# Kernel tuning notes

Hardware: AMD Instinct MI355X
Metric: run time of the kernel (lower is better)

The kernel has to match this reference:

```python
import jax, jax.numpy as jnp
import numpy as np

B, P = 16, 1024
D_TIME, NUM_MODS = 8, 22
DIM_S = NUM_MODS + D_TIME + 1  # 31
PHI_W, N_HEADS, DP = 32, 4, 32
PSI_W, PSI_L, RHO_W = 64, 64, 64
SQRT_DP = float(np.sqrt(DP))


def setup_inputs() -> dict:
    key = jax.random.key(0)
    ks = jax.random.split(key, 16)
    rn = lambda k, shape: jax.random.normal(k, shape, jnp.float32) * 0.05
    return dict(
        times=jax.random.uniform(ks[0], (B, P), jnp.float32) * 48.0,
        values=jax.random.normal(ks[1], (B, P), jnp.float32),
        measurements=jax.random.randint(ks[2], (B, P), 0, NUM_MODS + 1),
        non_pad_mask=jnp.ones((B, P, 1), jnp.float32),
        W_psi1=rn(ks[3], (DIM_S, PSI_W)), b_psi1=jnp.zeros((PSI_W,), jnp.float32),
        W_psi2=rn(ks[4], (PSI_W, PSI_L)), b_psi2=jnp.zeros((PSI_L,), jnp.float32),
        W_key=rn(ks[5], (DIM_S + PSI_L, N_HEADS * DP)), b_key=jnp.zeros((N_HEADS * DP,), jnp.float32),
        query=rn(ks[6], (N_HEADS, DP)),
        W_phi1=rn(ks[7], (DIM_S, PHI_W)), b_phi1=jnp.zeros((PHI_W,), jnp.float32),
        W_phi2=rn(ks[8], (PHI_W, PHI_W)), b_phi2=jnp.zeros((PHI_W,), jnp.float32),
        W_rho1=rn(ks[9], (N_HEADS * PHI_W, RHO_W)), b_rho1=jnp.zeros((RHO_W,), jnp.float32),
        W_rho2=rn(ks[10], (RHO_W, RHO_W)), b_rho2=jnp.zeros((RHO_W,), jnp.float32),
    )


def _temporal_enc(times):
    i = np.arange(D_TIME)
    pos_vec = jnp.asarray(10000.0 ** (2.0 * (i // 2) / D_TIME), jnp.float32)
    ang = times[:, :, None] / pos_vec  # [B,P,d_time]
    return jnp.where(jnp.asarray(i % 2 == 0), jnp.sin(ang), jnp.cos(ang))


def reference(times, values, measurements, non_pad_mask,
              W_psi1, b_psi1, W_psi2, b_psi2, W_key, b_key, query,
              W_phi1, b_phi1, W_phi2, b_phi2, W_rho1, b_rho1, W_rho2, b_rho2):
    m = non_pad_mask  # [B,P,1]
    te = _temporal_enc(times)
    oh = jax.nn.one_hot(measurements, NUM_MODS + 1, dtype=jnp.float32)[:, :, 1:]
    x = jnp.concatenate([te, values[:, :, None], oh], axis=-1)  # [B,P,dim_s]

    # CumulativeSetAttentionLayer: psi MLP -> cumulative mean -> keys . query
    psi = jax.nn.relu(jax.nn.relu(x @ W_psi1 + b_psi1) @ W_psi2 + b_psi2)  # [B,P,psi_l]
    cum = jnp.cumsum(psi * m, axis=1) / jnp.cumsum(m, axis=1)
    keys = (jnp.concatenate([x, cum], axis=-1) @ W_key + b_key).reshape(B, P, N_HEADS, DP)
    pre = jnp.einsum('bpmd,md->bpm', keys, query) / SQRT_DP  # [B,P,m]

    # phi MLP
    phi = jax.nn.relu(jax.nn.relu(x @ W_phi1 + b_phi1) @ W_phi2 + b_phi2) * m  # [B,P,phi_w]

    # cumulative softmax weighting (online path)
    cmax = jax.lax.cummax(pre, axis=1)  # [B,P,m], running max for stability
    D = jnp.exp(pre[:, None, :, :] - cmax[:, :, None, :])  # [B,P,Q,m]
    causal = jnp.arange(P)[:, None] >= jnp.arange(P)[None, :]  # keep Q <= P
    D = D * causal[None, :, :, None]
    E = D.sum(axis=2)  # [B,P,m]
    agg = jnp.einsum('bpqm,bqd->bpmd', D, phi) / E[:, :, :, None]
    agg = (agg * m[:, :, :, None]).reshape(B, P, N_HEADS * PHI_W)

    # rho MLP (return_sequences)
    out = jax.nn.relu(jax.nn.relu(agg @ W_rho1 + b_rho1) @ W_rho2 + b_rho2) * m
    return out
```

## Files before the change

kernel.cpp:

```cpp
#include <hip/hip_runtime.h>
#include <hip/hip_bf16.h>

#define B_ 16
#define P_ 1024
#define T_ (B_*P_)
#define CH_ 32
#define CL_ (P_/CH_)

constexpr int OFF_A     = 16;
constexpr int OFF_WPSI1 = 400;
constexpr int OFF_BPSI1 = OFF_WPSI1 + 1984;
constexpr int OFF_WPSI2 = OFF_BPSI1 + 64;
constexpr int OFF_BPSI2 = OFF_WPSI2 + 4096;
constexpr int OFF_WPHI1 = OFF_BPSI2 + 64;
constexpr int OFF_BPHI1 = OFF_WPHI1 + 992;
constexpr int OFF_WPHI2 = OFF_BPHI1 + 32;
constexpr int OFF_BPHI2 = OFF_WPHI2 + 1024;
constexpr int OFF_WRHO1 = OFF_BPHI2 + 32;
constexpr int OFF_BRHO1 = OFF_WRHO1 + 8192;
constexpr int OFF_WRHO2 = OFF_BRHO1 + 64;
constexpr int OFF_BRHO2 = OFF_WRHO2 + 4096;
constexpr int OFF_PHI   = OFF_BRHO2 + 64;
constexpr int OFF_Z     = OFF_PHI   + T_*32;
constexpr int OFF_PREX  = OFF_Z     + T_*4;
constexpr int OFF_EXPW  = OFF_PREX  + T_*4;
constexpr int OFF_CE    = OFF_EXPW  + T_*4;
constexpr int OFF_CS    = OFF_CE    + 2048;
constexpr int OFF_AGG   = OFF_CS    + 65536;

static __device__ __forceinline__ bool detect_f32(const void* mask_raw) {
  return ((*(const unsigned*)mask_raw) & 0xFFFFu) == 0u;
}
static __device__ __forceinline__ float ld_any(const void* src, int i, bool isf32) {
  if (isf32) return ((const float*)src)[i];
  return __bfloat162float(((const __hip_bfloat16*)src)[i]);
}

__global__ __launch_bounds__(256) void s01_prep(
    float* __restrict__ ws, const void* mask,
    const void* Wpsi1, const void* bpsi1, const void* Wpsi2, const void* bpsi2,
    const void* Wkey,  const void* bkey,  const void* query,
    const void* Wphi1, const void* bphi1, const void* Wphi2, const void* bphi2,
    const void* Wrho1, const void* brho1, const void* Wrho2, const void* brho2) {
  const bool isf32 = detect_f32(mask);
  if (blockIdx.x < 2) {
    const int gid = blockIdx.x * 256 + threadIdx.x;
    if (gid >= 384) return;
    const float inv_s = 0.17677669529663687f;
    const int h = gid & 3;
    const int j = gid >> 2;
    float s = 0.f;
    if (j < 95) {
      for (int d = 0; d < 32; ++d)
        s += ld_any(Wkey, j * 128 + h * 32 + d, isf32) * ld_any(query, h * 32 + d, isf32);
    } else {
      for (int d = 0; d < 32; ++d)
        s += ld_any(bkey, h * 32 + d, isf32) * ld_any(query, h * 32 + d, isf32);
    }
    ws[OFF_A + gid] = s * inv_s;
    return;
  }
  const int g  = (blockIdx.x - 2) * 256 + threadIdx.x;
  const int gs = (gridDim.x - 2) * 256;
  auto st = [&](int off, const void* src, int n) {
    for (int i = g; i < n; i += gs) ws[off + i] = ld_any(src, i, isf32);
  };
  st(OFF_WPSI1, Wpsi1, 1984); st(OFF_BPSI1, bpsi1, 64);
  st(OFF_WPSI2, Wpsi2, 4096); st(OFF_BPSI2, bpsi2, 64);
  st(OFF_WPHI1, Wphi1, 992);  st(OFF_BPHI1, bphi1, 32);
  st(OFF_WPHI2, Wphi2, 1024); st(OFF_BPHI2, bphi2, 32);
  st(OFF_WRHO1, Wrho1, 8192); st(OFF_BRHO1, brho1, 64);
  st(OFF_WRHO2, Wrho2, 4096); st(OFF_BRHO2, brho2, 64);
}

__global__ __launch_bounds__(256) void k1_token(float* __restrict__ ws,
                                                const int* __restrict__ measp,
                                                const void* __restrict__ times,
                                                const void* __restrict__ values,
                                                const void* __restrict__ mask) {
  __shared__ float sh1[4][64];
  __shared__ float sg1[4][32];
  const bool isf32 = detect_f32(mask);
  const int tid = threadIdx.x;
  const int wv  = __builtin_amdgcn_readfirstlane(tid >> 6);
  const int j   = tid & 63;
  const int t   = blockIdx.x * 4 + wv;

  const float tval = ld_any(times, t, isf32);
  const float vval = ld_any(values, t, isf32);
  const float mval = ld_any(mask, t, isf32);
  const int   meas = measp[t];
  const float sel  = (meas > 0) ? 1.f : 0.f;
  const int   mrow = (meas > 0) ? (8 + meas) : 0;

  float x[9];
  const float posv[4] = {1.f, 10.f, 100.f, 1000.f};
  #pragma unroll
  for (int k = 0; k < 4; ++k) {
    float s, c;
    __sincosf(tval / posv[k], &s, &c);
    x[2*k] = s; x[2*k+1] = c;
  }
  x[8] = vval;

  float h1 = ws[OFF_BPSI1 + j];
  #pragma unroll
  for (int i = 0; i < 9; ++i) h1 = fmaf(x[i], ws[OFF_WPSI1 + i * 64 + j], h1);
  h1 = fmaf(sel, ws[OFF_WPSI1 + mrow * 64 + j], h1);
  sh1[wv][j] = fmaxf(h1, 0.f);

  if (j < 32) {
    float g1 = ws[OFF_BPHI1 + j];
    #pragma unroll
    for (int i = 0; i < 9; ++i) g1 = fmaf(x[i], ws[OFF_WPHI1 + i * 32 + j], g1);
    g1 = fmaf(sel, ws[OFF_WPHI1 + mrow * 32 + j], g1);
    sg1[wv][j] = fmaxf(g1, 0.f);
  }
  __syncthreads();

  float h2 = ws[OFF_BPSI2 + j];
  #pragma unroll 8
  for (int i = 0; i < 64; ++i) h2 = fmaf(sh1[wv][i], ws[OFF_WPSI2 + i * 64 + j], h2);
  const float q = fmaxf(h2, 0.f) * mval;

  const float* a2 = ws + OFF_A + (31 + j) * 4;
  float z0 = q * a2[0], z1 = q * a2[1], z2 = q * a2[2], z3 = q * a2[3];
  #pragma unroll
  for (int off = 32; off; off >>= 1) {
    z0 += __shfl_xor(z0, off, 64);
    z1 += __shfl_xor(z1, off, 64);
    z2 += __shfl_xor(z2, off, 64);
    z3 += __shfl_xor(z3, off, 64);
  }
  if (j == 0) {
    float* zo = ws + OFF_Z + (size_t)t * 4;
    zo[0] = z0; zo[1] = z1; zo[2] = z2; zo[3] = z3;
  }

  if (j < 32) {
    float g2 = ws[OFF_BPHI2 + j];
    #pragma unroll 8
    for (int i = 0; i < 32; ++i) g2 = fmaf(sg1[wv][i], ws[OFF_WPHI2 + i * 32 + j], g2);
    ws[OFF_PHI + (size_t)t * 32 + j] = fmaxf(g2, 0.f) * mval;
  } else if (j < 36) {
    const int h = j - 32;
    float pr = ws[OFF_A + 380 + h];
    #pragma unroll
    for (int i = 0; i < 9; ++i) pr = fmaf(x[i], ws[OFF_A + i * 4 + h], pr);
    pr = fmaf(sel, ws[OFF_A + mrow * 4 + h], pr);
    ws[OFF_PREX + (size_t)t * 4 + h] = pr;
  }
}

__global__ __launch_bounds__(256) void k2_scanz(float* __restrict__ ws,
                                                const void* __restrict__ mask) {
  const int b   = blockIdx.x;
  const int tid = threadIdx.x;
  const bool isf32 = detect_f32(mask);
  __shared__ float sc[256], s0[256], s1[256], s2[256], s3[256];

  const float* zB = ws + OFF_Z + (size_t)b * P_ * 4;
  const int p0 = tid * 4;

  float lc[4], l0[4], l1[4], l2[4], l3[4];
  float c = 0.f, z0 = 0.f, z1 = 0.f, z2 = 0.f, z3 = 0.f;
  #pragma unroll
  for (int i = 0; i < 4; ++i) {
    c  += ld_any(mask, b * P_ + p0 + i, isf32);
    z0 += zB[(p0 + i) * 4 + 0]; z1 += zB[(p0 + i) * 4 + 1];
    z2 += zB[(p0 + i) * 4 + 2]; z3 += zB[(p0 + i) * 4 + 3];
    lc[i] = c; l0[i] = z0; l1[i] = z1; l2[i] = z2; l3[i] = z3;
  }

  float rc = c, r0 = z0, r1 = z1, r2 = z2, r3 = z3;
  sc[tid] = rc; s0[tid] = r0; s1[tid] = r1; s2[tid] = r2; s3[tid] = r3;
  __syncthreads();
  for (int off = 1; off < 256; off <<= 1) {
    float ac = 0.f, a0 = 0.f, a1 = 0.f, a2 = 0.f, a3 = 0.f;
    if (tid >= off) {
      ac = sc[tid - off]; a0 = s0[tid - off]; a1 = s1[tid - off];
      a2 = s2[tid - off]; a3 = s3[tid - off];
    }
    __syncthreads();
    rc += ac; r0 += a0; r1 += a1; r2 += a2; r3 += a3;
    sc[tid] = rc; s0[tid] = r0; s1[tid] = r1; s2[tid] = r2; s3[tid] = r3;
    __syncthreads();
  }
  const float ec = rc - c, e0 = r0 - z0, e1 = r1 - z1, e2 = r2 - z2, e3 = r3 - z3;

  const float* px = ws + OFF_PREX + (size_t)b * P_ * 4;
  float pre[4][4];
  float mx0 = -1e30f, mx1 = -1e30f, mx2 = -1e30f, mx3 = -1e30f;
  #pragma unroll
  for (int i = 0; i < 4; ++i) {
    const float inv = 1.f / (ec + lc[i]);
    const int p = p0 + i;
    pre[i][0] = px[p * 4 + 0] + (e0 + l0[i]) * inv;
    pre[i][1] = px[p * 4 + 1] + (e1 + l1[i]) * inv;
    pre[i][2] = px[p * 4 + 2] + (e2 + l2[i]) * inv;
    pre[i][3] = px[p * 4 + 3] + (e3 + l3[i]) * inv;
    mx0 = fmaxf(mx0, pre[i][0]); mx1 = fmaxf(mx1, pre[i][1]);
    mx2 = fmaxf(mx2, pre[i][2]); mx3 = fmaxf(mx3, pre[i][3]);
  }

  __syncthreads();
  s0[tid] = mx0; s1[tid] = mx1; s2[tid] = mx2; s3[tid] = mx3;
  __syncthreads();
  for (int off = 128; off; off >>= 1) {
    if (tid < off) {
      s0[tid] = fmaxf(s0[tid], s0[tid + off]);
      s1[tid] = fmaxf(s1[tid], s1[tid + off]);
      s2[tid] = fmaxf(s2[tid], s2[tid + off]);
      s3[tid] = fmaxf(s3[tid], s3[tid + off]);
    }
    __syncthreads();
  }
  const float M0 = s0[0], M1 = s1[0], M2 = s2[0], M3 = s3[0];

  float* eB = ws + OFF_EXPW + (size_t)b * P_ * 4;
  #pragma unroll
  for (int i = 0; i < 4; ++i) {
    const int p = p0 + i;
    eB[p * 4 + 0] = __expf(pre[i][0] - M0);
    eB[p * 4 + 1] = __expf(pre[i][1] - M1);
    eB[p * 4 + 2] = __expf(pre[i][2] - M2);
    eB[p * 4 + 3] = __expf(pre[i][3] - M3);
  }
}

__global__ __launch_bounds__(128) void k4a_sums(float* __restrict__ ws) {
  const int ch = blockIdx.x, b = blockIdx.y;
  const int h = threadIdx.x >> 5, d = threadIdx.x & 31;
  const float* eB   = ws + OFF_EXPW + (size_t)b * P_ * 4;
  const float* phiB = ws + OFF_PHI  + (size_t)b * P_ * 32;

  float E = 0.f, S = 0.f;
  const int pbeg = ch * CL_;
  #pragma unroll 4
  for (int p = pbeg; p < pbeg + CL_; ++p) {
    const float e  = eB[p * 4 + h];
    const float ph = phiB[p * 32 + d];
    E += e;
    S = fmaf(e, ph, S);
  }
  const int base = (b * CH_ + ch) * 4 + h;
  if (d == 0) ws[OFF_CE + base] = E;
  ws[OFF_CS + base * 32 + d] = S;
}

__global__ __launch_bounds__(128) void k4c_replay(float* __restrict__ ws,
                                                  const void* __restrict__ mask) {
  const int ch = blockIdx.x, b = blockIdx.y;
  const int h = threadIdx.x >> 5, d = threadIdx.x & 31;
  const bool isf32 = detect_f32(mask);
  const float* eB   = ws + OFF_EXPW + (size_t)b * P_ * 4;
  const float* phiB = ws + OFF_PHI  + (size_t)b * P_ * 32;
  float*       aggB = ws + OFF_AGG  + (size_t)b * P_ * 128;

  float E = 0.f, S = 0.f;
  for (int c2 = 0; c2 < ch; ++c2) {
    const int base2 = (b * CH_ + c2) * 4 + h;
    E += ws[OFF_CE + base2];
    S += ws[OFF_CS + base2 * 32 + d];
  }

  const int pbeg = ch * CL_;
  for (int p = pbeg; p < pbeg + CL_; ++p) {
    const float e  = eB[p * 4 + h];
    const float ph = phiB[p * 32 + d];
    E += e;
    S = fmaf(e, ph, S);
    aggB[p * 128 + h * 32 + d] = (S / E) * ld_any(mask, b * P_ + p, isf32);
  }
}

__global__ __launch_bounds__(256) void k5_rho(const float* __restrict__ ws,
                                              const void* __restrict__ mask_raw,
                                              void* __restrict__ out) {
  __shared__ float sW1[128 * 64];
  __shared__ float sH1[16][64];
  const int tid = threadIdx.x;
  for (int i = tid; i < 128 * 64; i += 256) sW1[i] = ws[OFF_WRHO1 + i];

  const int wv = __builtin_amdgcn_readfirstlane(tid >> 6);
  const int j  = tid & 63;
  const int t0 = blockIdx.x * 16 + wv * 4;
  const float* aggB = ws + OFF_AGG;

  const float b1 = ws[OFF_BRHO1 + j];
  float a0 = b1, a1 = b1, a2 = b1, a3 = b1;
  __syncthreads();

  #pragma unroll 8
  for (int i = 0; i < 128; ++i) {
    const float w = sW1[i * 64 + j];
    a0 = fmaf(aggB[(size_t)(t0 + 0) * 128 + i], w, a0);
    a1 = fmaf(aggB[(size_t)(t0 + 1) * 128 + i], w, a1);
    a2 = fmaf(aggB[(size_t)(t0 + 2) * 128 + i], w, a2);
    a3 = fmaf(aggB[(size_t)(t0 + 3) * 128 + i], w, a3);
  }
  sH1[wv * 4 + 0][j] = fmaxf(a0, 0.f);
  sH1[wv * 4 + 1][j] = fmaxf(a1, 0.f);
  sH1[wv * 4 + 2][j] = fmaxf(a2, 0.f);
  sH1[wv * 4 + 3][j] = fmaxf(a3, 0.f);
  __syncthreads();

  const float b2 = ws[OFF_BRHO2 + j];
  float o0 = b2, o1 = b2, o2 = b2, o3 = b2;
  #pragma unroll 8
  for (int i = 0; i < 64; ++i) {
    const float w = ws[OFF_WRHO2 + i * 64 + j];
    o0 = fmaf(sH1[wv * 4 + 0][i], w, o0);
    o1 = fmaf(sH1[wv * 4 + 1][i], w, o1);
    o2 = fmaf(sH1[wv * 4 + 2][i], w, o2);
    o3 = fmaf(sH1[wv * 4 + 3][i], w, o3);
  }

  const bool isf32 = detect_f32(mask_raw);
  float r[4] = {o0, o1, o2, o3};
  #pragma unroll
  for (int k = 0; k < 4; ++k) {
    const int t = t0 + k;
    const float v = fmaxf(r[k], 0.f) * ld_any(mask_raw, t, isf32);
    if (isf32) {
      ((float*)out)[(size_t)t * 64 + j] = v;
    } else {
      ((__hip_bfloat16*)out)[(size_t)t * 64 + j] = __float2bfloat16(v);
    }
  }
}

extern "C" void kernel_launch(void* const* d_in, const int* in_sizes, int n_in,
                              void* d_out, int out_size, void* d_ws, size_t ws_size,
                              hipStream_t stream) {
  const int* meas = (const int*)d_in[2];
  const void* times = d_in[0];
  const void* values = d_in[1];
  const void* mask = d_in[3];
  float* ws = (float*)d_ws;

  s01_prep<<<34, 256, 0, stream>>>(ws, mask,
                                   d_in[4], d_in[5], d_in[6], d_in[7],
                                   d_in[8], d_in[9], d_in[10],
                                   d_in[11], d_in[12], d_in[13], d_in[14],
                                   d_in[15], d_in[16], d_in[17], d_in[18]);
  k1_token<<<T_/4, 256, 0, stream>>>(ws, meas, times, values, mask);
  k2_scanz<<<B_, 256, 0, stream>>>(ws, mask);
  k4a_sums<<<dim3(CH_, B_), 128, 0, stream>>>(ws);
  k4c_replay<<<dim3(CH_, B_), 128, 0, stream>>>(ws, mask);
  k5_rho<<<T_/16, 256, 0, stream>>>(ws, mask, d_out);
}
```

Before: 160.3 us.

## Fuse chunk replay scan into rho MLP kernel, keeping agg in shared memory

Drops the separate replay kernel that wrote the full aggregated tensor to global memory. Each rho block now recomputes the prefix state for its 16 tokens from the chunk sums and scans locally into shared memory. Half the threads copy the rho weights with float4 loads while the other half run the scan. This removes a kernel launch and a large global write and read round trip. In exchange it does redundant scan work, since later blocks in a chunk replay up to 32 positions and sum up to 31 prior chunks.

```diff
diff --git a/kernel.cpp b/kernel.cpp
--- a/kernel.cpp
+++ b/kernel.cpp
@@ -26,7 +26,6 @@
 constexpr int OFF_EXPW  = OFF_PREX  + T_*4;
 constexpr int OFF_CE    = OFF_EXPW  + T_*4;
 constexpr int OFF_CS    = OFF_CE    + 2048;
-constexpr int OFF_AGG   = OFF_CS    + 65536;
 
 static __device__ __forceinline__ bool detect_f32(const void* mask_raw) {
   return ((*(const unsigned*)mask_raw) & 0xFFFFu) == 0u;
@@ -248,61 +247,66 @@
   ws[OFF_CS + base * 32 + d] = S;
 }
 
-__global__ __launch_bounds__(128) void k4c_replay(float* __restrict__ ws,
-                                                  const void* __restrict__ mask) {
-  const int ch = blockIdx.x, b = blockIdx.y;
-  const int h = threadIdx.x >> 5, d = threadIdx.x & 31;
-  const bool isf32 = detect_f32(mask);
-  const float* eB   = ws + OFF_EXPW + (size_t)b * P_ * 4;
-  const float* phiB = ws + OFF_PHI  + (size_t)b * P_ * 32;
-  float*       aggB = ws + OFF_AGG  + (size_t)b * P_ * 128;
-
-  float E = 0.f, S = 0.f;
-  for (int c2 = 0; c2 < ch; ++c2) {
-    const int base2 = (b * CH_ + c2) * 4 + h;
-    E += ws[OFF_CE + base2];
-    S += ws[OFF_CS + base2 * 32 + d];
-  }
-
-  const int pbeg = ch * CL_;
-  for (int p = pbeg; p < pbeg + CL_; ++p) {
-    const float e  = eB[p * 4 + h];
-    const float ph = phiB[p * 32 + d];
-    E += e;
-    S = fmaf(e, ph, S);
-    aggB[p * 128 + h * 32 + d] = (S / E) * ld_any(mask, b * P_ + p, isf32);
-  }
-}
-
-__global__ __launch_bounds__(256) void k5_rho(const float* __restrict__ ws,
-                                              const void* __restrict__ mask_raw,
-                                              void* __restrict__ out) {
+__global__ __launch_bounds__(256) void k5_fused(float* __restrict__ ws,
+                                                const void* __restrict__ mask_raw,
+                                                void* __restrict__ out) {
+  __shared__ float sAgg[16][128];
   __shared__ float sW1[128 * 64];
   __shared__ float sH1[16][64];
   const int tid = threadIdx.x;
-  for (int i = tid; i < 128 * 64; i += 256) sW1[i] = ws[OFF_WRHO1 + i];
+  const bool isf32 = detect_f32(mask_raw);
+
+  const int tg0  = blockIdx.x * 16;
+  const int b    = tg0 >> 10;
+  const int p0   = tg0 & (P_ - 1);
+  const int ch   = p0 >> 5;
+  const int pbeg = ch * CL_;
+
+  if (tid < 128) {
+    const int h = tid >> 5, d = tid & 31;
+    const float* eB   = ws + OFF_EXPW + (size_t)b * P_ * 4;
+    const float* phiB = ws + OFF_PHI  + (size_t)b * P_ * 32;
+    float E = 0.f, S = 0.f;
+    for (int c2 = 0; c2 < ch; ++c2) {
+      const int base2 = (b * CH_ + c2) * 4 + h;
+      E += ws[OFF_CE + base2];
+      S += ws[OFF_CS + base2 * 32 + d];
+    }
+    for (int p = pbeg; p < p0 + 16; ++p) {
+      const float e  = eB[p * 4 + h];
+      const float ph = phiB[p * 32 + d];
+      E += e;
+      S = fmaf(e, ph, S);
+      if (p >= p0)
+        sAgg[p - p0][tid] = (S / E) * ld_any(mask_raw, b * P_ + p, isf32);
+    }
+  } else {
+    const int t2 = tid - 128;
+    const float4* src = (const float4*)(ws + OFF_WRHO1);
+    float4* dst = (float4*)sW1;
+    #pragma unroll
+    for (int k = 0; k < 16; ++k) dst[t2 + k * 128] = src[t2 + k * 128];
+  }
+  __syncthreads();
 
   const int wv = __builtin_amdgcn_readfirstlane(tid >> 6);
   const int j  = tid & 63;
-  const int t0 = blockIdx.x * 16 + wv * 4;
-  const float* aggB = ws + OFF_AGG;
+  const int l0 = wv * 4;
 
   const float b1 = ws[OFF_BRHO1 + j];
   float a0 = b1, a1 = b1, a2 = b1, a3 = b1;
-  __syncthreads();
-
   #pragma unroll 8
   for (int i = 0; i < 128; ++i) {
     const float w = sW1[i * 64 + j];
-    a0 = fmaf(aggB[(size_t)(t0 + 0) * 128 + i], w, a0);
-    a1 = fmaf(aggB[(size_t)(t0 + 1) * 128 + i], w, a1);
-    a2 = fmaf(aggB[(size_t)(t0 + 2) * 128 + i], w, a2);
-    a3 = fmaf(aggB[(size_t)(t0 + 3) * 128 + i], w, a3);
-  }
-  sH1[wv * 4 + 0][j] = fmaxf(a0, 0.f);
-  sH1[wv * 4 + 1][j] = fmaxf(a1, 0.f);
-  sH1[wv * 4 + 2][j] = fmaxf(a2, 0.f);
-  sH1[wv * 4 + 3][j] = fmaxf(a3, 0.f);
+    a0 = fmaf(sAgg[l0 + 0][i], w, a0);
+    a1 = fmaf(sAgg[l0 + 1][i], w, a1);
+    a2 = fmaf(sAgg[l0 + 2][i], w, a2);
+    a3 = fmaf(sAgg[l0 + 3][i], w, a3);
+  }
+  sH1[l0 + 0][j] = fmaxf(a0, 0.f);
+  sH1[l0 + 1][j] = fmaxf(a1, 0.f);
+  sH1[l0 + 2][j] = fmaxf(a2, 0.f);
+  sH1[l0 + 3][j] = fmaxf(a3, 0.f);
   __syncthreads();
 
   const float b2 = ws[OFF_BRHO2 + j];
@@ -310,17 +314,16 @@
   #pragma unroll 8
   for (int i = 0; i < 64; ++i) {
     const float w = ws[OFF_WRHO2 + i * 64 + j];
-    o0 = fmaf(sH1[wv * 4 + 0][i], w, o0);
-    o1 = fmaf(sH1[wv * 4 + 1][i], w, o1);
-    o2 = fmaf(sH1[wv * 4 + 2][i], w, o2);
-    o3 = fmaf(sH1[wv * 4 + 3][i], w, o3);
-  }
-
-  const bool isf32 = detect_f32(mask_raw);
-  float r[4] = {o0, o1, o2, o3};
+    o0 = fmaf(sH1[l0 + 0][i], w, o0);
+    o1 = fmaf(sH1[l0 + 1][i], w, o1);
+    o2 = fmaf(sH1[l0 + 2][i], w, o2);
+    o3 = fmaf(sH1[l0 + 3][i], w, o3);
+  }
+
+  const float r[4] = {o0, o1, o2, o3};
   #pragma unroll
   for (int k = 0; k < 4; ++k) {
-    const int t = t0 + k;
+    const int t = tg0 + l0 + k;
     const float v = fmaxf(r[k], 0.f) * ld_any(mask_raw, t, isf32);
     if (isf32) {
       ((float*)out)[(size_t)t * 64 + j] = v;
@@ -347,6 +350,5 @@
   k1_token<<<T_/4, 256, 0, stream>>>(ws, meas, times, values, mask);
   k2_scanz<<<B_, 256, 0, stream>>>(ws, mask);
   k4a_sums<<<dim3(CH_, B_), 128, 0, stream>>>(ws);
-  k4c_replay<<<dim3(CH_, B_), 128, 0, stream>>>(ws, mask);
-  k5_rho<<<T_/16, 256, 0, stream>>>(ws, mask, d_out);
-}
+  k5_fused<<<T_/16, 256, 0, stream>>>(ws, mask, d_out);
+}
```

New measurement: 173.7 us. +8.3%, slower.
